# Kernel optimization log

Measured on AMD Instinct MI355X. Metric: run time of the kernel, lower is better.

The kernel has to match this reference:

```python
import jax, jax.numpy as jnp
import numpy as np

B, T, H = 8, 4096, 1024
K, V = 128, 128
OUT = 1024

def setup_inputs() -> dict:
    key = jax.random.key(0)
    k1, k2, k3, k4, k5 = jax.random.split(key, 5)
    s = 1.0 / np.sqrt(H)
    return {
        "hidden_state": jax.random.normal(k1, (B, T, H), dtype=jnp.float32),
        "W_proj": jax.random.normal(k2, (H, 3 * K + V), dtype=jnp.float32) * s,
        "b_proj": jax.random.normal(k3, (3 * K + V,), dtype=jnp.float32) * 0.01,
        "W_out": jax.random.normal(k4, (V, OUT), dtype=jnp.float32) * (1.0 / np.sqrt(V)),
        "b_out": jax.random.normal(k5, (OUT,), dtype=jnp.float32) * 0.01,
    }

def reference(hidden_state, W_proj, b_proj, W_out, b_out):
    # fused projection over all timesteps at once: (B,T,3K+V)
    qkgv = jnp.einsum("bth,hd->btd", hidden_state, W_proj) + b_proj
    q, k, g, v = jnp.split(qkgv, [K, 2 * K, 3 * K], axis=-1)
    k = jax.nn.sigmoid(k)
    g = jax.nn.sigmoid(g)

    # time-major for scan: (T,B,*)
    xs = (jnp.swapaxes(q, 0, 1), jnp.swapaxes(k, 0, 1),
          jnp.swapaxes(g, 0, 1), jnp.swapaxes(v, 0, 1))
    cell0 = jnp.zeros((B, K, V), dtype=hidden_state.dtype)

    def step(cell, x):
        q_i, k_i, g_i, v_i = x
        # gated outer-product state update: cell (B,K,V)
        cell = cell * g_i[:, :, None] + k_i[:, :, None] * v_i[:, None, :]
        # query readout: (B,V)
        o_i = jnp.einsum("bkv,bk->bv", cell, q_i)
        return cell, o_i

    final_state, outs = jax.lax.scan(step, cell0, xs)
    outputs = jnp.swapaxes(outs, 0, 1)  # (B,T,V)
    outputs = jnp.einsum("btv,vo->bto", outputs, W_out) + b_out
    return outputs, final_state
```

## Files before the change

kernel.cpp:

```cpp
#include <hip/hip_runtime.h>
#include <math.h>

#define B_ 8
#define T_ 4096
#define H_ 1024
#define K_ 128
#define V_ 128
#define OUT_ 1024
#define NPROJ 512
#define M_ (B_*T_)
#define CC 32
#define NC 128

typedef __attribute__((ext_vector_type(8))) short bf16x8;
typedef __attribute__((ext_vector_type(4))) float f32x4;

__device__ inline unsigned short f2bf(float f){
  union{float f; unsigned int u;} x; x.f = f;
  unsigned int r = x.u + 0x7fff + ((x.u>>16)&1);
  return (unsigned short)(r>>16);
}
__device__ inline float bf2f(unsigned short u){
  union{unsigned int i; float f;} x; x.i = ((unsigned int)u)<<16; return x.f;
}

#define GL16(gp, lp) __builtin_amdgcn_global_load_lds(\
  (const __attribute__((address_space(1))) unsigned int*)(gp), \
  (__attribute__((address_space(3))) unsigned int*)(lp), 16, 0, 0)

#define MFMA16(a,b,c) __builtin_amdgcn_mfma_f32_16x16x32_bf16((a),(b),(c),0,0,0)

__global__ __launch_bounds__(256)
void convT(const float* __restrict__ src, unsigned short* __restrict__ dst,
           int Kd, int N) {
  __shared__ float t[32][33];
  int tx = threadIdx.x & 31, ty = threadIdx.x >> 5;
  int n0 = blockIdx.x * 32, k0 = blockIdx.y * 32;
  #pragma unroll
  for (int r=0;r<4;r++){
    int k = ty*4 + r;
    t[k][tx] = src[(long)(k0+k)*N + n0 + tx];
  }
  __syncthreads();
  #pragma unroll
  for (int r=0;r<4;r++){
    int n = ty*4 + r;
    dst[(long)(n0+n)*Kd + k0 + tx] = f2bf(t[tx][n]);
  }
}

__global__ __launch_bounds__(512, 4)
void proj_mfma4(const float* __restrict__ A, const unsigned short* __restrict__ Bt,
                const float* __restrict__ bias,
                unsigned short* __restrict__ qbf, unsigned short* __restrict__ kbf,
                float* __restrict__ gf, unsigned short* __restrict__ vbf) {
  __shared__ unsigned short sA[128*72];
  __shared__ unsigned short sB[256*64];
  int tid = threadIdx.x, lane = tid & 63, wid = tid >> 6;
  int wm = wid >> 2, wn = wid & 3;
  int l16 = lane & 15, g8 = (lane >> 4) * 8;
  long row0 = (long)blockIdx.y * 128;
  int col0 = blockIdx.x * 256;

  int arow = tid >> 2, acol0 = (tid & 3) * 16;
  const float* Ab = A + (row0 + arow) * 1024 + acol0;
  int srowB = lane >> 3;
  int scolB = (((lane & 7) ^ (srowB & 7)) * 8);

  f32x4 acc[4][4];
  #pragma unroll
  for (int i=0;i<4;i++)
    #pragma unroll
    for (int j=0;j<4;j++) acc[i][j] = (f32x4){0.f,0.f,0.f,0.f};

  float4 ra[4];
  #define LDA(k0_) { _Pragma("unroll") \
    for (int j_=0;j_<4;j_++) ra[j_] = *(const float4*)(Ab + (k0_) + j_*4); }
  #define STA() { \
    unsigned short o_[16]; \
    _Pragma("unroll") \
    for (int j_=0;j_<4;j_++){ \
      o_[j_*4+0]=f2bf(ra[j_].x); o_[j_*4+1]=f2bf(ra[j_].y); \
      o_[j_*4+2]=f2bf(ra[j_].z); o_[j_*4+3]=f2bf(ra[j_].w); \
    } \
    *(uint4*)&sA[arow*72 + acol0]     = ((uint4*)o_)[0]; \
    *(uint4*)&sA[arow*72 + acol0 + 8] = ((uint4*)o_)[1]; \
  }
  #define STB(k0_) { _Pragma("unroll") \
    for (int i_=0;i_<4;i_++){ \
      int r_ = wid*32 + i_*8; \
      GL16(Bt + (long)(col0 + r_ + srowB)*1024 + (k0_) + scolB, &sB[r_*64]); \
    } }

  LDA(0);
  for (int t = 0; t < 16; ++t) {
    STA();
    STB(t*64);
    __syncthreads();
    if (t < 15) { LDA(t*64 + 64); }
    #pragma unroll
    for (int kk2 = 0; kk2 < 2; ++kk2) {
      int kk = kk2 * 32;
      bf16x8 af[4], bf[4];
      #pragma unroll
      for (int mi=0;mi<4;mi++)
        af[mi] = *(const bf16x8*)&sA[(wm*64 + mi*16 + l16)*72 + kk + g8];
      #pragma unroll
      for (int ni=0;ni<4;ni++){
        int brow = wn*64 + ni*16 + l16;
        int slot = ((kk + g8) >> 3) ^ (brow & 7);
        bf[ni] = *(const bf16x8*)&sB[brow*64 + slot*8];
      }
      #pragma unroll
      for (int mi=0;mi<4;mi++)
        #pragma unroll
        for (int ni=0;ni<4;ni++)
          acc[mi][ni] = MFMA16(af[mi], bf[ni], acc[mi][ni]);
    }
    __syncthreads();
  }
  #undef LDA
  #undef STA
  #undef STB

  int seg = blockIdx.x*2 + (wn>>1);
  int cbase = (wn&1)*64;
  #pragma unroll
  for (int mi=0;mi<4;mi++){
    #pragma unroll
    for (int ni=0;ni<4;ni++){
      int c = cbase + ni*16 + l16;
      float bsv = bias[seg*128 + c];
      #pragma unroll
      for (int r=0;r<4;r++){
        long grow = row0 + wm*64 + mi*16 + (lane>>4)*4 + r;
        float v = acc[mi][ni][r] + bsv;
        long off = grow*128 + c;
        if (seg == 0)      qbf[off] = f2bf(v);
        else if (seg == 1) kbf[off] = f2bf(1.f/(1.f+__expf(-v)));
        else if (seg == 2) gf[off]  = 1.f/(1.f+__expf(-v));
        else               vbf[off] = f2bf(v);
      }
    }
  }
}

__global__ __launch_bounds__(128)
void prep(const float* __restrict__ gf, unsigned short* __restrict__ qbf,
          unsigned short* __restrict__ kbf, const unsigned short* __restrict__ vbf,
          unsigned short* __restrict__ khT, unsigned short* __restrict__ vT,
          float* __restrict__ Gc) {
  int k = threadIdx.x;
  int c = blockIdx.x, b = blockIdx.y;
  long base = ((long)b*T_ + (long)c*CC) * 128;
  float G = 1.f;
  float kt[CC];
  unsigned short vv[CC];
  #pragma unroll
  for (int t=0;t<CC;++t){
    long off = base + (long)t*128 + k;
    float g = gf[off];
    G *= g;
    float q = bf2f(qbf[off]);
    qbf[off] = f2bf(q*G);
    float kk = bf2f(kbf[off]);
    float ktl = kk/G;
    kbf[off] = f2bf(ktl);
    kt[t] = ktl;
    vv[t] = vbf[off];
  }
  long cb = (long)b*NC + c;
  Gc[cb*128 + k] = G;
  unsigned short ob[CC];
  #pragma unroll
  for (int s=0;s<CC;++s) ob[s] = f2bf(kt[s]*G);
  long tbase = (cb*128 + k)*CC;
  #pragma unroll
  for (int j=0;j<4;j++) *(uint4*)(khT + tbase + j*8) = *(uint4*)(ob + j*8);
  #pragma unroll
  for (int j=0;j<4;j++) *(uint4*)(vT + tbase + j*8) = *(uint4*)(vv + j*8);
}

__global__ __launch_bounds__(256)
void chunkstate(const unsigned short* __restrict__ khT, const unsigned short* __restrict__ vT,
                unsigned short* __restrict__ Ut) {
  __shared__ unsigned short kS[128][36];
  __shared__ unsigned short vS[128][36];
  int tid = threadIdx.x, lane = tid&63, w = tid>>6;
  long cb = (long)blockIdx.y*NC + blockIdx.x;
  const unsigned short* kg = khT + cb*4096;
  const unsigned short* vg = vT  + cb*4096;
  #pragma unroll
  for (int j=0;j<2;j++){
    int idx = tid + j*256;
    int r = idx>>2, s8 = (idx&3)*8;
    *(uint4*)&kS[r][s8] = *(const uint4*)(kg + r*32 + s8);
    *(uint4*)&vS[r][s8] = *(const uint4*)(vg + r*32 + s8);
  }
  __syncthreads();
  int l16 = lane&15, g8 = (lane>>4)*8;
  bf16x8 af[2], bfr[8];
  #pragma unroll
  for (int i=0;i<2;i++) af[i] = *(const bf16x8*)&vS[w*32 + i*16 + l16][g8];
  #pragma unroll
  for (int j=0;j<8;j++) bfr[j] = *(const bf16x8*)&kS[j*16 + l16][g8];
  #pragma unroll
  for (int i=0;i<2;i++){
    #pragma unroll
    for (int j=0;j<8;j++){
      f32x4 acc = (f32x4){0.f,0.f,0.f,0.f};
      acc = MFMA16(af[i], bfr[j], acc);
      int kcol = j*16 + l16;
      #pragma unroll
      for (int r=0;r<4;r++){
        int vrow = w*32 + i*16 + (lane>>4)*4 + r;
        Ut[cb*16384 + vrow*128 + kcol] = f2bf(acc[r]);
      }
    }
  }
}

__global__ __launch_bounds__(256)
void seqstate_a(const float* __restrict__ Gc, const unsigned short* __restrict__ Ut,
                float* __restrict__ segB, float* __restrict__ segG) {
  int idx = blockIdx.x*256 + threadIdx.x;
  int s = blockIdx.y, b = blockIdx.z;
  int v = idx>>5, k0 = (idx&31)*4;
  float cell[4] = {0.f,0.f,0.f,0.f};
  float gp[4] = {1.f,1.f,1.f,1.f};
  long ub = (long)b*NC*16384 + (long)v*128 + k0;
  long gb = (long)b*NC*128 + k0;
  int c0 = s*16;
  #pragma unroll 4
  for (int c=c0; c<c0+16; ++c){
    uint2 u = *(const uint2*)(Ut + ub + (long)c*16384);
    float4 gc = *(const float4*)(Gc + gb + (long)c*128);
    cell[0] = fmaf(cell[0], gc.x, bf2f((unsigned short)(u.x & 0xffff)));
    cell[1] = fmaf(cell[1], gc.y, bf2f((unsigned short)(u.x >> 16)));
    cell[2] = fmaf(cell[2], gc.z, bf2f((unsigned short)(u.y & 0xffff)));
    cell[3] = fmaf(cell[3], gc.w, bf2f((unsigned short)(u.y >> 16)));
    gp[0] *= gc.x; gp[1] *= gc.y; gp[2] *= gc.z; gp[3] *= gc.w;
  }
  long sb = ((long)b*8 + s)*16384 + (long)v*128 + k0;
  *(float4*)(segB + sb) = make_float4(cell[0],cell[1],cell[2],cell[3]);
  if (v == 0)
    *(float4*)(segG + ((long)b*8 + s)*128 + k0) = make_float4(gp[0],gp[1],gp[2],gp[3]);
}

__global__ __launch_bounds__(256)
void seqstate_b(const float* __restrict__ Gc, unsigned short* __restrict__ Ut,
                const float* __restrict__ segB, const float* __restrict__ segG,
                float* __restrict__ fstate) {
  int idx = blockIdx.x*256 + threadIdx.x;
  int s = blockIdx.y, b = blockIdx.z;
  int v = idx>>5, k0 = (idx&31)*4;
  float cell[4] = {0.f,0.f,0.f,0.f};
  for (int sp=0; sp<s; ++sp){
    float4 bg = *(const float4*)(segG + ((long)b*8 + sp)*128 + k0);
    float4 bb = *(const float4*)(segB + ((long)b*8 + sp)*16384 + (long)v*128 + k0);
    cell[0] = fmaf(cell[0], bg.x, bb.x);
    cell[1] = fmaf(cell[1], bg.y, bb.y);
    cell[2] = fmaf(cell[2], bg.z, bb.z);
    cell[3] = fmaf(cell[3], bg.w, bb.w);
  }
  long ub = (long)b*NC*16384 + (long)v*128 + k0;
  long gb = (long)b*NC*128 + k0;
  int c0 = s*16;
  #pragma unroll 4
  for (int c=c0; c<c0+16; ++c){
    uint2 u = *(const uint2*)(Ut + ub + (long)c*16384);
    float4 gc = *(const float4*)(Gc + gb + (long)c*128);
    unsigned short cb4[4] = {f2bf(cell[0]), f2bf(cell[1]), f2bf(cell[2]), f2bf(cell[3])};
    *(uint2*)(Ut + ub + (long)c*16384) = *(uint2*)cb4;
    cell[0] = fmaf(cell[0], gc.x, bf2f((unsigned short)(u.x & 0xffff)));
    cell[1] = fmaf(cell[1], gc.y, bf2f((unsigned short)(u.x >> 16)));
    cell[2] = fmaf(cell[2], gc.z, bf2f((unsigned short)(u.y & 0xffff)));
    cell[3] = fmaf(cell[3], gc.w, bf2f((unsigned short)(u.y >> 16)));
  }
  if (s == 7){
    #pragma unroll
    for (int j=0;j<4;j++)
      fstate[((long)b*128 + k0 + j)*128 + v] = cell[j];
  }
}

#define CP 140
__global__ __launch_bounds__(256)
void chunkout(const unsigned short* __restrict__ qbf, const unsigned short* __restrict__ kbf,
              const unsigned short* __restrict__ vT, const unsigned short* __restrict__ cellT,
              unsigned short* __restrict__ obf) {
  __shared__ unsigned short qS[32][CP];
  __shared__ unsigned short kS[32][CP];
  __shared__ unsigned short cS[128][CP];
  __shared__ unsigned short vS[128][36];
  __shared__ unsigned short pS[4][32][36];
  int tid = threadIdx.x, lane = tid&63, w = tid>>6;
  long cb = (long)blockIdx.y*NC + blockIdx.x;
  const unsigned short* qg = qbf + cb*4096;
  const unsigned short* kg = kbf + cb*4096;
  const unsigned short* vg = vT  + cb*4096;
  const unsigned short* cg = cellT + cb*16384;
  #pragma unroll
  for (int j=0;j<2;j++){
    int idx = tid + j*256;
    int r = idx>>4, c8 = (idx&15)*8;
    *(uint4*)&qS[r][c8] = *(const uint4*)(qg + r*128 + c8);
    *(uint4*)&kS[r][c8] = *(const uint4*)(kg + r*128 + c8);
    int rv = idx>>2, s8 = (idx&3)*8;
    *(uint4*)&vS[rv][s8] = *(const uint4*)(vg + rv*32 + s8);
  }
  #pragma unroll
  for (int j=0;j<8;j++){
    int idx = tid + j*256;
    int r = idx>>4, c8 = (idx&15)*8;
    *(uint4*)&cS[r][c8] = *(const uint4*)(cg + r*128 + c8);
  }
  __syncthreads();

  int l16 = lane&15, g = lane>>4, g8 = g*8;
  f32x4 s00 = (f32x4){0.f,0.f,0.f,0.f}, s01 = s00, s11 = s00;
  #pragma unroll
  for (int ks=0; ks<4; ++ks){
    bf16x8 ka = *(const bf16x8*)&kS[l16][ks*32+g8];
    bf16x8 kb = *(const bf16x8*)&kS[16+l16][ks*32+g8];
    bf16x8 qa = *(const bf16x8*)&qS[l16][ks*32+g8];
    bf16x8 qb = *(const bf16x8*)&qS[16+l16][ks*32+g8];
    s00 = MFMA16(ka, qa, s00);
    s01 = MFMA16(ka, qb, s01);
    s11 = MFMA16(kb, qb, s11);
  }
  pS[w][l16][16 + 4*g + (0)] = 0; pS[w][l16][16 + 4*g + 1] = 0;
  pS[w][l16][16 + 4*g + 2] = 0;   pS[w][l16][16 + 4*g + 3] = 0;
  #pragma unroll
  for (int r=0;r<4;r++){
    int sl = 4*g + r;
    pS[w][l16][sl]       = (l16 >= sl) ? f2bf(s00[r]) : (unsigned short)0;
    pS[w][16+l16][sl]    = f2bf(s01[r]);
    pS[w][16+l16][16+sl] = (l16 >= sl) ? f2bf(s11[r]) : (unsigned short)0;
  }
  f32x4 o[2][2];
  #pragma unroll
  for (int i=0;i<2;i++)
    #pragma unroll
    for (int j=0;j<2;j++) o[i][j] = (f32x4){0.f,0.f,0.f,0.f};
  {
    bf16x8 p0 = *(const bf16x8*)&pS[w][l16][g8];
    bf16x8 p1 = *(const bf16x8*)&pS[w][16+l16][g8];
    bf16x8 v0 = *(const bf16x8*)&vS[w*32 + l16][g8];
    bf16x8 v1 = *(const bf16x8*)&vS[w*32 + 16 + l16][g8];
    o[0][0] = MFMA16(p0, v0, o[0][0]);
    o[0][1] = MFMA16(p0, v1, o[0][1]);
    o[1][0] = MFMA16(p1, v0, o[1][0]);
    o[1][1] = MFMA16(p1, v1, o[1][1]);
  }
  #pragma unroll
  for (int ks=0; ks<4; ++ks){
    bf16x8 qa = *(const bf16x8*)&qS[l16][ks*32+g8];
    bf16x8 qb = *(const bf16x8*)&qS[16+l16][ks*32+g8];
    bf16x8 c0 = *(const bf16x8*)&cS[w*32 + l16][ks*32+g8];
    bf16x8 c1 = *(const bf16x8*)&cS[w*32 + 16 + l16][ks*32+g8];
    o[0][0] = MFMA16(qa, c0, o[0][0]);
    o[0][1] = MFMA16(qa, c1, o[0][1]);
    o[1][0] = MFMA16(qb, c0, o[1][0]);
    o[1][1] = MFMA16(qb, c1, o[1][1]);
  }
  #pragma unroll
  for (int ti=0;ti<2;ti++)
    #pragma unroll
    for (int vi=0;vi<2;vi++)
      #pragma unroll
      for (int r=0;r<4;r++){
        int t = ti*16 + 4*g + r;
        int v = w*32 + vi*16 + l16;
        obf[cb*4096 + (long)t*128 + v] = f2bf(o[ti][vi][r]);
      }
}

__global__ __launch_bounds__(256)
void out_mfma(const unsigned short* __restrict__ A, const unsigned short* __restrict__ Bt,
              const float* __restrict__ bias, float* __restrict__ C) {
  __shared__ unsigned short As[128*32];
  __shared__ unsigned short Bs[128*32];
  int tid = threadIdx.x, lane = tid & 63, wid = tid >> 6;
  long row0 = (long)blockIdx.y * 128;
  int col0 = blockIdx.x * 128;
  f32x4 acc[4][4];
  #pragma unroll
  for (int i=0;i<4;i++)
    #pragma unroll
    for (int j=0;j<4;j++) acc[i][j] = (f32x4){0.f,0.f,0.f,0.f};

  const unsigned short* Ab = A + row0*128;
  const unsigned short* Bb = Bt + (long)col0*128;
  int srow = lane >> 2;
  int soff = (lane & 3) * 8;
  int wrow = (wid>>1)*64, wcol = (wid&1)*64;

  for (int k0 = 0; k0 < 128; k0 += 32) {
    #pragma unroll
    for (int i=0;i<2;i++){
      int r = wid*32 + i*16;
      GL16(Ab + (long)(r + srow)*128 + k0 + soff, &As[r*32]);
      GL16(Bb + (long)(r + srow)*128 + k0 + soff, &Bs[r*32]);
    }
    __syncthreads();
    bf16x8 af[4], bfr[4];
    #pragma unroll
    for (int mi=0;mi<4;mi++)
      af[mi] = *(const bf16x8*)&As[(wrow + mi*16 + (lane&15))*32 + (lane>>4)*8];
    #pragma unroll
    for (int ni=0;ni<4;ni++)
      bfr[ni] = *(const bf16x8*)&Bs[(wcol + ni*16 + (lane&15))*32 + (lane>>4)*8];
    #pragma unroll
    for (int mi=0;mi<4;mi++)
      #pragma unroll
      for (int ni=0;ni<4;ni++)
        acc[mi][ni] = MFMA16(af[mi], bfr[ni], acc[mi][ni]);
    __syncthreads();
  }

  #pragma unroll
  for (int mi=0;mi<4;mi++){
    #pragma unroll
    for (int ni=0;ni<4;ni++){
      int col = col0 + wcol + ni*16 + (lane&15);
      float bsv = bias[col];
      #pragma unroll
      for (int r=0;r<4;r++){
        long grow = row0 + wrow + mi*16 + (lane>>4)*4 + r;
        C[grow*OUT_ + col] = acc[mi][ni][r] + bsv;
      }
    }
  }
}

extern "C" void kernel_launch(void* const* d_in, const int* in_sizes, int n_in,
                              void* d_out, int out_size, void* d_ws, size_t ws_size,
                              hipStream_t stream) {
  const float* hidden = (const float*)d_in[0];
  const float* Wp     = (const float*)d_in[1];
  const float* bp     = (const float*)d_in[2];
  const float* Wo     = (const float*)d_in[3];
  const float* bo     = (const float*)d_in[4];
  float* out    = (float*)d_out;
  float* fstate = out + (long)M_ * OUT_;

  char* w = (char*)d_ws;
  unsigned short* khT   = (unsigned short*)w;
  unsigned short* vT    = (unsigned short*)(w + 8388608);
  float*          Gc    = (float*)(w + 16777216);
  unsigned short* Ut    = (unsigned short*)(w + 17301504);
  unsigned short* obf   = (unsigned short*)(w + 50855936);
  float*          segB  = (float*)(w + 59244544);
  float*          segG  = (float*)(w + 63438848);
  unsigned short* Wot = (unsigned short*)(w + 67108864);
  unsigned short* Wpt = (unsigned short*)(w + 67371008);
  unsigned short* qbf = (unsigned short*)(w + 68419584);
  unsigned short* kbf = (unsigned short*)(w + 76808192);
  unsigned short* vbf = (unsigned short*)(w + 85196800);
  float*          gf  = (float*)(w + 93585408);

  convT<<<dim3(NPROJ/32, H_/32), 256, 0, stream>>>(Wp, Wpt, H_, NPROJ);
  convT<<<dim3(OUT_/32, V_/32), 256, 0, stream>>>(Wo, Wot, V_, OUT_);
  proj_mfma4<<<dim3(2, 256), 512, 0, stream>>>(hidden, Wpt, bp, qbf, kbf, gf, vbf);
  prep<<<dim3(NC, B_), 128, 0, stream>>>(gf, qbf, kbf, vbf, khT, vT, Gc);
  chunkstate<<<dim3(NC, B_), 256, 0, stream>>>(khT, vT, Ut);
  seqstate_a<<<dim3(16, 8, B_), 256, 0, stream>>>(Gc, Ut, segB, segG);
  seqstate_b<<<dim3(16, 8, B_), 256, 0, stream>>>(Gc, Ut, segB, segG, fstate);
  chunkout<<<dim3(NC, B_), 256, 0, stream>>>(qbf, kbf, vT, Ut, obf);
  out_mfma<<<dim3(8, 256), 256, 0, stream>>>(obf, Wot, bo, out);
}
```

Measured before the change: 180.2 us.

## Double-buffer A tile in projection GEMM with manual waitcnt barriers

The projection GEMM now keeps two LDS buffers for the converted A tile and holds two register sets of prefetched fp32 A data, so global loads run two tiles ahead of the MFMA work. Full __syncthreads pairs are replaced by explicit s_waitcnt vmcnt(4) plus s_barrier, with scheduling barriers to pin the instruction order. The A-load pattern also changes to strided float4 columns, which gives a different coalescing and LDS store layout. This relies on a hand-set vmcnt count that assumes a fixed number of outstanding loads, and the extra buffers raise LDS and register use.

```diff
diff --git a/kernel.cpp b/kernel.cpp
--- a/kernel.cpp
+++ b/kernel.cpp
@@ -50,11 +50,11 @@
 }
 
 __global__ __launch_bounds__(512, 4)
-void proj_mfma4(const float* __restrict__ A, const unsigned short* __restrict__ Bt,
+void proj_mfma8(const float* __restrict__ A, const unsigned short* __restrict__ Bt,
                 const float* __restrict__ bias,
                 unsigned short* __restrict__ qbf, unsigned short* __restrict__ kbf,
                 float* __restrict__ gf, unsigned short* __restrict__ vbf) {
-  __shared__ unsigned short sA[128*72];
+  __shared__ unsigned short sA[2][128*72];
   __shared__ unsigned short sB[256*64];
   int tid = threadIdx.x, lane = tid & 63, wid = tid >> 6;
   int wm = wid >> 2, wn = wid & 3;
@@ -62,10 +62,10 @@
   long row0 = (long)blockIdx.y * 128;
   int col0 = blockIdx.x * 256;
 
-  int arow = tid >> 2, acol0 = (tid & 3) * 16;
+  int arow = tid >> 2, acol0 = (tid & 3) * 4;
   const float* Ab = A + (row0 + arow) * 1024 + acol0;
   int srowB = lane >> 3;
-  int scolB = (((lane & 7) ^ (srowB & 7)) * 8);
+  int scolB = ((lane & 7) ^ srowB) * 8;
 
   f32x4 acc[4][4];
   #pragma unroll
@@ -73,55 +73,75 @@
     #pragma unroll
     for (int j=0;j<4;j++) acc[i][j] = (f32x4){0.f,0.f,0.f,0.f};
 
-  float4 ra[4];
-  #define LDA(k0_) { _Pragma("unroll") \
-    for (int j_=0;j_<4;j_++) ra[j_] = *(const float4*)(Ab + (k0_) + j_*4); }
-  #define STA() { \
-    unsigned short o_[16]; \
-    _Pragma("unroll") \
+  float4 rE[4], rO[4];
+
+  #define SFENCE __builtin_amdgcn_sched_barrier(0)
+  #define LDA(dst_, k0_) { _Pragma("unroll") \
+    for (int j_=0;j_<4;j_++) dst_[j_] = *(const float4*)(Ab + (k0_) + j_*16); }
+  #define STA(bi_, src_) { _Pragma("unroll") \
     for (int j_=0;j_<4;j_++){ \
-      o_[j_*4+0]=f2bf(ra[j_].x); o_[j_*4+1]=f2bf(ra[j_].y); \
-      o_[j_*4+2]=f2bf(ra[j_].z); o_[j_*4+3]=f2bf(ra[j_].w); \
-    } \
-    *(uint4*)&sA[arow*72 + acol0]     = ((uint4*)o_)[0]; \
-    *(uint4*)&sA[arow*72 + acol0 + 8] = ((uint4*)o_)[1]; \
-  }
+      unsigned short o_[4] = {f2bf(src_[j_].x), f2bf(src_[j_].y), \
+                              f2bf(src_[j_].z), f2bf(src_[j_].w)}; \
+      *(uint2*)&sA[bi_][arow*72 + acol0 + j_*16] = *(uint2*)o_; \
+    } }
   #define STB(k0_) { _Pragma("unroll") \
     for (int i_=0;i_<4;i_++){ \
       int r_ = wid*32 + i_*8; \
       GL16(Bt + (long)(col0 + r_ + srowB)*1024 + (k0_) + scolB, &sB[r_*64]); \
     } }
-
-  LDA(0);
-  for (int t = 0; t < 16; ++t) {
-    STA();
-    STB(t*64);
-    __syncthreads();
-    if (t < 15) { LDA(t*64 + 64); }
-    #pragma unroll
-    for (int kk2 = 0; kk2 < 2; ++kk2) {
-      int kk = kk2 * 32;
-      bf16x8 af[4], bf[4];
-      #pragma unroll
-      for (int mi=0;mi<4;mi++)
-        af[mi] = *(const bf16x8*)&sA[(wm*64 + mi*16 + l16)*72 + kk + g8];
-      #pragma unroll
-      for (int ni=0;ni<4;ni++){
-        int brow = wn*64 + ni*16 + l16;
-        int slot = ((kk + g8) >> 3) ^ (brow & 7);
-        bf[ni] = *(const bf16x8*)&sB[brow*64 + slot*8];
-      }
-      #pragma unroll
-      for (int mi=0;mi<4;mi++)
-        #pragma unroll
-        for (int ni=0;ni<4;ni++)
-          acc[mi][ni] = MFMA16(af[mi], bf[ni], acc[mi][ni]);
-    }
-    __syncthreads();
-  }
+  #define FRAGS(bi_) { _Pragma("unroll") \
+    for (int kk2_=0;kk2_<2;kk2_++){ int kk_ = kk2_*32; \
+      _Pragma("unroll") \
+      for (int mi_=0;mi_<4;mi_++) \
+        af[kk2_][mi_] = *(const bf16x8*)&sA[bi_][(wm*64 + mi_*16 + l16)*72 + kk_ + g8]; \
+      _Pragma("unroll") \
+      for (int ni_=0;ni_<4;ni_++){ \
+        int brow_ = wn*64 + ni_*16 + l16; \
+        int slot_ = ((kk_ + g8) >> 3) ^ (brow_ & 7); \
+        bf[kk2_][ni_] = *(const bf16x8*)&sB[brow_*64 + slot_*8]; \
+      } \
+    } }
+  #define MFMAS { _Pragma("unroll") \
+    for (int kk2_=0;kk2_<2;kk2_++) \
+      _Pragma("unroll") \
+      for (int mi_=0;mi_<4;mi_++) \
+        _Pragma("unroll") \
+        for (int ni_=0;ni_<4;ni_++) \
+          acc[mi_][ni_] = MFMA16(af[kk2_][mi_], bf[kk2_][ni_], acc[mi_][ni_]); }
+  #define BARV4 { asm volatile("s_waitcnt vmcnt(4) lgkmcnt(0)" ::: "memory"); \
+    SFENCE; __builtin_amdgcn_s_barrier(); SFENCE; }
+  #define BARX  { SFENCE; __builtin_amdgcn_s_barrier(); SFENCE; }
+
+  bf16x8 af[2][4], bf[2][4];
+
+  LDA(rE, 0);    SFENCE;
+  STA(0, rE);    SFENCE;
+  LDA(rE, 64);   SFENCE;
+  LDA(rO, 128);  SFENCE;
+
+  for (int t2 = 0; t2 < 16; t2 += 2) {
+    STB(t2*64);              SFENCE;
+    STA(1, rE);              SFENCE;
+    { int kn = (t2+3 > 15) ? 15 : t2+3; LDA(rE, kn*64); } SFENCE;
+    BARV4;
+    FRAGS(0); MFMAS;
+    BARX;
+    STB((t2+1)*64);          SFENCE;
+    if (t2+1 < 15) { STA(0, rO); SFENCE; }
+    { int kn = (t2+4 > 15) ? 15 : t2+4; LDA(rO, kn*64); } SFENCE;
+    BARV4;
+    FRAGS(1); MFMAS;
+    BARX;
+  }
+
+  #undef SFENCE
   #undef LDA
   #undef STA
   #undef STB
+  #undef FRAGS
+  #undef MFMAS
+  #undef BARV4
+  #undef BARX
 
   int seg = blockIdx.x*2 + (wn>>1);
   int cbase = (wn&1)*64;
@@ -462,7 +482,7 @@
 
   convT<<<dim3(NPROJ/32, H_/32), 256, 0, stream>>>(Wp, Wpt, H_, NPROJ);
   convT<<<dim3(OUT_/32, V_/32), 256, 0, stream>>>(Wo, Wot, V_, OUT_);
-  proj_mfma4<<<dim3(2, 256), 512, 0, stream>>>(hidden, Wpt, bp, qbf, kbf, gf, vbf);
+  proj_mfma8<<<dim3(2, 256), 512, 0, stream>>>(hidden, Wpt, bp, qbf, kbf, gf, vbf);
   prep<<<dim3(NC, B_), 128, 0, stream>>>(gf, qbf, kbf, vbf, khT, vT, Gc);
   chunkstate<<<dim3(NC, B_), 256, 0, stream>>>(khT, vT, Ut);
   seqstate_a<<<dim3(16, 8, B_), 256, 0, stream>>>(Gc, Ut, segB, segG);
```

Result: slower. 297.4 us (+65.1%).

## Fuse prep into chunkstate, chunkout into output GEMM, merge weight transposes

Applied to the files above, without the earlier changes.

Merges the two weight-transpose launches into one, fuses the per-chunk gate prefix/scaling pass with the chunk state MFMA (keys and values staged directly in LDS, with the 32-step gate product split across two thread halves), and fuses the chunk readout with the output projection so the bf16 intermediate outputs never go to global memory. This removes launches and the khT/obf round trips. In exchange, the output GEMM now runs on only 1024 blocks with 32-row tiles and reads W_out fragments straight from global/L2 with no LDS reuse, which may lower MFMA efficiency compared with the separate tiled GEMM.

```diff
diff --git a/kernel.cpp b/kernel.cpp
--- a/kernel.cpp
+++ b/kernel.cpp
@@ -31,11 +31,16 @@
 #define MFMA16(a,b,c) __builtin_amdgcn_mfma_f32_16x16x32_bf16((a),(b),(c),0,0,0)
 
 __global__ __launch_bounds__(256)
-void convT(const float* __restrict__ src, unsigned short* __restrict__ dst,
-           int Kd, int N) {
+void convT2(const float* __restrict__ Wp, const float* __restrict__ Wo,
+            unsigned short* __restrict__ Wpt, unsigned short* __restrict__ Wot) {
   __shared__ float t[32][33];
   int tx = threadIdx.x & 31, ty = threadIdx.x >> 5;
-  int n0 = blockIdx.x * 32, k0 = blockIdx.y * 32;
+  const float* src; unsigned short* dst; int Kd, N, n0, k0;
+  int bid = blockIdx.x;
+  if (bid < 512) { src = Wp; dst = Wpt; Kd = 1024; N = 512;
+    n0 = (bid & 15)*32; k0 = (bid >> 4)*32; }
+  else { int j = bid - 512; src = Wo; dst = Wot; Kd = 128; N = 1024;
+    n0 = (j & 31)*32; k0 = (j >> 5)*32; }
   #pragma unroll
   for (int r=0;r<4;r++){
     int k = ty*4 + r;
@@ -145,60 +150,59 @@
   }
 }
 
-__global__ __launch_bounds__(128)
-void prep(const float* __restrict__ gf, unsigned short* __restrict__ qbf,
-          unsigned short* __restrict__ kbf, const unsigned short* __restrict__ vbf,
-          unsigned short* __restrict__ khT, unsigned short* __restrict__ vT,
-          float* __restrict__ Gc) {
-  int k = threadIdx.x;
-  int c = blockIdx.x, b = blockIdx.y;
-  long base = ((long)b*T_ + (long)c*CC) * 128;
-  float G = 1.f;
-  float kt[CC];
-  unsigned short vv[CC];
-  #pragma unroll
-  for (int t=0;t<CC;++t){
-    long off = base + (long)t*128 + k;
-    float g = gf[off];
-    G *= g;
-    float q = bf2f(qbf[off]);
-    qbf[off] = f2bf(q*G);
-    float kk = bf2f(kbf[off]);
-    float ktl = kk/G;
-    kbf[off] = f2bf(ktl);
-    kt[t] = ktl;
-    vv[t] = vbf[off];
-  }
-  long cb = (long)b*NC + c;
-  Gc[cb*128 + k] = G;
-  unsigned short ob[CC];
-  #pragma unroll
-  for (int s=0;s<CC;++s) ob[s] = f2bf(kt[s]*G);
-  long tbase = (cb*128 + k)*CC;
-  #pragma unroll
-  for (int j=0;j<4;j++) *(uint4*)(khT + tbase + j*8) = *(uint4*)(ob + j*8);
-  #pragma unroll
-  for (int j=0;j<4;j++) *(uint4*)(vT + tbase + j*8) = *(uint4*)(vv + j*8);
-}
-
 __global__ __launch_bounds__(256)
-void chunkstate(const unsigned short* __restrict__ khT, const unsigned short* __restrict__ vT,
-                unsigned short* __restrict__ Ut) {
+void prep_cs(const float* __restrict__ gf, unsigned short* __restrict__ qbf,
+             unsigned short* __restrict__ kbf, const unsigned short* __restrict__ vbf,
+             unsigned short* __restrict__ vT, float* __restrict__ Gc,
+             unsigned short* __restrict__ Ut) {
   __shared__ unsigned short kS[128][36];
   __shared__ unsigned short vS[128][36];
-  int tid = threadIdx.x, lane = tid&63, w = tid>>6;
-  long cb = (long)blockIdx.y*NC + blockIdx.x;
-  const unsigned short* kg = khT + cb*4096;
-  const unsigned short* vg = vT  + cb*4096;
-  #pragma unroll
-  for (int j=0;j<2;j++){
-    int idx = tid + j*256;
-    int r = idx>>2, s8 = (idx&3)*8;
-    *(uint4*)&kS[r][s8] = *(const uint4*)(kg + r*32 + s8);
-    *(uint4*)&vS[r][s8] = *(const uint4*)(vg + r*32 + s8);
-  }
-  __syncthreads();
-  int l16 = lane&15, g8 = (lane>>4)*8;
+  __shared__ float gtot[2][128];
+  int tid = threadIdx.x;
+  int c = blockIdx.x, b = blockIdx.y;
+  int k = tid & 127, half = tid >> 7;
+  long base = ((long)b*T_ + (long)c*CC + half*16) * 128;
+
+  float gloc[16];
+  {
+    float G = 1.f;
+    #pragma unroll
+    for (int t=0;t<16;++t){
+      G *= gf[base + (long)t*128 + k];
+      gloc[t] = G;
+    }
+    gtot[half][k] = G;
+  }
+  __syncthreads();
+  float pre  = half ? gtot[0][k] : 1.f;
+  float Gtot = gtot[0][k] * gtot[1][k];
+
+  unsigned short kh[16], vv[16];
+  #pragma unroll
+  for (int t=0;t<16;++t){
+    long off = base + (long)t*128 + k;
+    float Gt = pre * gloc[t];
+    float q = bf2f(qbf[off]);
+    qbf[off] = f2bf(q*Gt);
+    float kk = bf2f(kbf[off]);
+    float ktl = kk/Gt;
+    kbf[off] = f2bf(ktl);
+    kh[t] = f2bf(ktl*Gtot);
+    vv[t] = vbf[off];
+  }
+  *(uint4*)&kS[k][half*16]   = ((uint4*)kh)[0];
+  *(uint4*)&kS[k][half*16+8] = ((uint4*)kh)[1];
+  *(uint4*)&vS[k][half*16]   = ((uint4*)vv)[0];
+  *(uint4*)&vS[k][half*16+8] = ((uint4*)vv)[1];
+  long cb = (long)b*NC + c;
+  if (half == 0) Gc[cb*128 + k] = Gtot;
+  long tb = (cb*128 + k)*CC + half*16;
+  *(uint4*)(vT + tb)     = ((uint4*)vv)[0];
+  *(uint4*)(vT + tb + 8) = ((uint4*)vv)[1];
+  __syncthreads();
+
+  int lane = tid & 63, w = tid >> 6;
+  int l16 = lane & 15, g8 = (lane >> 4) * 8;
   bf16x8 af[2], bfr[8];
   #pragma unroll
   for (int i=0;i<2;i++) af[i] = *(const bf16x8*)&vS[w*32 + i*16 + l16][g8];
@@ -286,14 +290,16 @@
 
 #define CP 140
 __global__ __launch_bounds__(256)
-void chunkout(const unsigned short* __restrict__ qbf, const unsigned short* __restrict__ kbf,
-              const unsigned short* __restrict__ vT, const unsigned short* __restrict__ cellT,
-              unsigned short* __restrict__ obf) {
+void chunkout_out(const unsigned short* __restrict__ qbf, const unsigned short* __restrict__ kbf,
+                  const unsigned short* __restrict__ vT, const unsigned short* __restrict__ cellT,
+                  const unsigned short* __restrict__ Wot, const float* __restrict__ bo,
+                  float* __restrict__ out) {
   __shared__ unsigned short qS[32][CP];
   __shared__ unsigned short kS[32][CP];
   __shared__ unsigned short cS[128][CP];
   __shared__ unsigned short vS[128][36];
   __shared__ unsigned short pS[4][32][36];
+  unsigned short (*oS)[144] = (unsigned short (*)[144])&pS[0][0][0];
   int tid = threadIdx.x, lane = tid&63, w = tid>>6;
   long cb = (long)blockIdx.y*NC + blockIdx.x;
   const unsigned short* qg = qbf + cb*4096;
@@ -329,8 +335,8 @@
     s01 = MFMA16(ka, qb, s01);
     s11 = MFMA16(kb, qb, s11);
   }
-  pS[w][l16][16 + 4*g + (0)] = 0; pS[w][l16][16 + 4*g + 1] = 0;
-  pS[w][l16][16 + 4*g + 2] = 0;   pS[w][l16][16 + 4*g + 3] = 0;
+  pS[w][l16][16 + 4*g + 0] = 0; pS[w][l16][16 + 4*g + 1] = 0;
+  pS[w][l16][16 + 4*g + 2] = 0; pS[w][l16][16 + 4*g + 3] = 0;
   #pragma unroll
   for (int r=0;r<4;r++){
     int sl = 4*g + r;
@@ -364,73 +370,48 @@
     o[1][0] = MFMA16(qb, c0, o[1][0]);
     o[1][1] = MFMA16(qb, c1, o[1][1]);
   }
+  __syncthreads();
   #pragma unroll
   for (int ti=0;ti<2;ti++)
     #pragma unroll
     for (int vi=0;vi<2;vi++)
       #pragma unroll
-      for (int r=0;r<4;r++){
-        int t = ti*16 + 4*g + r;
-        int v = w*32 + vi*16 + l16;
-        obf[cb*4096 + (long)t*128 + v] = f2bf(o[ti][vi][r]);
-      }
-}
-
-__global__ __launch_bounds__(256)
-void out_mfma(const unsigned short* __restrict__ A, const unsigned short* __restrict__ Bt,
-              const float* __restrict__ bias, float* __restrict__ C) {
-  __shared__ unsigned short As[128*32];
-  __shared__ unsigned short Bs[128*32];
-  int tid = threadIdx.x, lane = tid & 63, wid = tid >> 6;
-  long row0 = (long)blockIdx.y * 128;
-  int col0 = blockIdx.x * 128;
-  f32x4 acc[4][4];
-  #pragma unroll
-  for (int i=0;i<4;i++)
-    #pragma unroll
-    for (int j=0;j<4;j++) acc[i][j] = (f32x4){0.f,0.f,0.f,0.f};
-
-  const unsigned short* Ab = A + row0*128;
-  const unsigned short* Bb = Bt + (long)col0*128;
-  int srow = lane >> 2;
-  int soff = (lane & 3) * 8;
-  int wrow = (wid>>1)*64, wcol = (wid&1)*64;
-
-  for (int k0 = 0; k0 < 128; k0 += 32) {
-    #pragma unroll
-    for (int i=0;i<2;i++){
-      int r = wid*32 + i*16;
-      GL16(Ab + (long)(r + srow)*128 + k0 + soff, &As[r*32]);
-      GL16(Bb + (long)(r + srow)*128 + k0 + soff, &Bs[r*32]);
-    }
-    __syncthreads();
-    bf16x8 af[4], bfr[4];
-    #pragma unroll
-    for (int mi=0;mi<4;mi++)
-      af[mi] = *(const bf16x8*)&As[(wrow + mi*16 + (lane&15))*32 + (lane>>4)*8];
-    #pragma unroll
-    for (int ni=0;ni<4;ni++)
-      bfr[ni] = *(const bf16x8*)&Bs[(wcol + ni*16 + (lane&15))*32 + (lane>>4)*8];
-    #pragma unroll
-    for (int mi=0;mi<4;mi++)
-      #pragma unroll
-      for (int ni=0;ni<4;ni++)
-        acc[mi][ni] = MFMA16(af[mi], bfr[ni], acc[mi][ni]);
-    __syncthreads();
-  }
-
-  #pragma unroll
-  for (int mi=0;mi<4;mi++){
-    #pragma unroll
-    for (int ni=0;ni<4;ni++){
-      int col = col0 + wcol + ni*16 + (lane&15);
-      float bsv = bias[col];
-      #pragma unroll
-      for (int r=0;r<4;r++){
-        long grow = row0 + wrow + mi*16 + (lane>>4)*4 + r;
-        C[grow*OUT_ + col] = acc[mi][ni][r] + bsv;
+      for (int r=0;r<4;r++)
+        oS[ti*16 + 4*g + r][w*32 + vi*16 + l16] = f2bf(o[ti][vi][r]);
+  __syncthreads();
+
+  long rowb = (long)blockIdx.y*T_ + (long)blockIdx.x*CC;
+  #pragma unroll
+  for (int nh=0; nh<2; ++nh){
+    f32x4 oc[2][8];
+    #pragma unroll
+    for (int mt=0;mt<2;mt++)
+      #pragma unroll
+      for (int nt=0;nt<8;nt++) oc[mt][nt] = (f32x4){0.f,0.f,0.f,0.f};
+    #pragma unroll
+    for (int ks=0; ks<4; ++ks){
+      bf16x8 a0 = *(const bf16x8*)&oS[l16][ks*32+g8];
+      bf16x8 a1 = *(const bf16x8*)&oS[16+l16][ks*32+g8];
+      #pragma unroll
+      for (int nt=0; nt<8; ++nt){
+        int n = w*256 + nh*128 + nt*16 + l16;
+        bf16x8 bw = *(const bf16x8*)(Wot + (long)n*128 + ks*32 + g8);
+        oc[0][nt] = MFMA16(a0, bw, oc[0][nt]);
+        oc[1][nt] = MFMA16(a1, bw, oc[1][nt]);
       }
     }
+    #pragma unroll
+    for (int mt=0; mt<2; ++mt)
+      #pragma unroll
+      for (int nt=0; nt<8; ++nt){
+        int col = w*256 + nh*128 + nt*16 + l16;
+        float bv = bo[col];
+        #pragma unroll
+        for (int r=0;r<4;r++){
+          long row = rowb + mt*16 + g*4 + r;
+          out[row*OUT_ + col] = oc[mt][nt][r] + bv;
+        }
+      }
   }
 }
 
@@ -446,13 +427,11 @@
   float* fstate = out + (long)M_ * OUT_;
 
   char* w = (char*)d_ws;
-  unsigned short* khT   = (unsigned short*)w;
-  unsigned short* vT    = (unsigned short*)(w + 8388608);
-  float*          Gc    = (float*)(w + 16777216);
-  unsigned short* Ut    = (unsigned short*)(w + 17301504);
-  unsigned short* obf   = (unsigned short*)(w + 50855936);
-  float*          segB  = (float*)(w + 59244544);
-  float*          segG  = (float*)(w + 63438848);
+  unsigned short* vT    = (unsigned short*)w;
+  float*          Gc    = (float*)(w + 8388608);
+  unsigned short* Ut    = (unsigned short*)(w + 8912896);
+  float*          segB  = (float*)(w + 42467328);
+  float*          segG  = (float*)(w + 46661632);
   unsigned short* Wot = (unsigned short*)(w + 67108864);
   unsigned short* Wpt = (unsigned short*)(w + 67371008);
   unsigned short* qbf = (unsigned short*)(w + 68419584);
@@ -460,13 +439,10 @@
   unsigned short* vbf = (unsigned short*)(w + 85196800);
   float*          gf  = (float*)(w + 93585408);
 
-  convT<<<dim3(NPROJ/32, H_/32), 256, 0, stream>>>(Wp, Wpt, H_, NPROJ);
-  convT<<<dim3(OUT_/32, V_/32), 256, 0, stream>>>(Wo, Wot, V_, OUT_);
+  convT2<<<640, 256, 0, stream>>>(Wp, Wo, Wpt, Wot);
   proj_mfma4<<<dim3(2, 256), 512, 0, stream>>>(hidden, Wpt, bp, qbf, kbf, gf, vbf);
-  prep<<<dim3(NC, B_), 128, 0, stream>>>(gf, qbf, kbf, vbf, khT, vT, Gc);
-  chunkstate<<<dim3(NC, B_), 256, 0, stream>>>(khT, vT, Ut);
+  prep_cs<<<dim3(NC, B_), 256, 0, stream>>>(gf, qbf, kbf, vbf, vT, Gc, Ut);
   seqstate_a<<<dim3(16, 8, B_), 256, 0, stream>>>(Gc, Ut, segB, segG);
   seqstate_b<<<dim3(16, 8, B_), 256, 0, stream>>>(Gc, Ut, segB, segG, fstate);
-  chunkout<<<dim3(NC, B_), 256, 0, stream>>>(qbf, kbf, vT, Ut, obf);
-  out_mfma<<<dim3(8, 256), 256, 0, stream>>>(obf, Wot, bo, out);
-}
+  chunkout_out<<<dim3(NC, B_), 256, 0, stream>>>(qbf, kbf, vT, Ut, Wot, bo, out);
+}
```

Measured after the change: 177.9 us. About the same (-1.3%).
